# Kernel tuning notes

Measured on AMD Instinct MI355X. Metric: run time of the kernel, lower is better.

The kernel has to match this reference:

```python
import jax, jax.numpy as jnp
import numpy as np

DN = ('NCHW', 'OIHW', 'NCHW')

def conv(x, w, b, stride, pad):
    y = jax.lax.conv_general_dilated(x, w, (stride, stride), ((pad, pad), (pad, pad)), dimension_numbers=DN)
    return y + b[None, :, None, None]

def conv_transpose(x, w, b, stride, pad):
    # w has torch ConvTranspose2d layout (Cin, Cout, kh, kw)
    k = w.shape[2]
    w_f = jnp.transpose(w[:, :, ::-1, ::-1], (1, 0, 2, 3))  # -> OIHW, spatially flipped
    p = k - 1 - pad
    y = jax.lax.conv_general_dilated(x, w_f, (1, 1), ((p, p), (p, p)), lhs_dilation=(stride, stride), dimension_numbers=DN)
    return y + b[None, :, None, None]

def setup_inputs() -> dict:
    key = jax.random.key(0)
    ks = jax.random.split(key, 16)
    K, D = 512, 64
    s = 0.05
    inp = {
        'x': jax.random.uniform(ks[0], (32, 3, 256, 256), dtype=jnp.float32),
        'enc_w1': jax.random.normal(ks[1], (32, 3, 4, 4), jnp.float32) * s,
        'enc_b1': jnp.zeros((32,), jnp.float32),
        'enc_w2': jax.random.normal(ks[2], (64, 32, 4, 4), jnp.float32) * s,
        'enc_b2': jnp.zeros((64,), jnp.float32),
        'enc_w3': jax.random.normal(ks[3], (D, 64, 3, 3), jnp.float32) * s,
        'enc_b3': jnp.zeros((D,), jnp.float32),
        'codebook': jax.random.uniform(ks[4], (K, D), jnp.float32, -1.0 / K, 1.0 / K),
        'dec_w1': jax.random.normal(ks[5], (D, 64, 4, 4), jnp.float32) * s,   # ConvT (Cin,Cout,k,k)
        'dec_b1': jnp.zeros((64,), jnp.float32),
        'dec_w2': jax.random.normal(ks[6], (64, 32, 4, 4), jnp.float32) * s,  # ConvT
        'dec_b2': jnp.zeros((32,), jnp.float32),
        'dec_w3': jax.random.normal(ks[7], (3, 32, 3, 3), jnp.float32) * s,
        'dec_b3': jnp.zeros((3,), jnp.float32),
    }
    return inp

COMMITMENT_COST = 0.25

def reference(x, enc_w1, enc_b1, enc_w2, enc_b2, enc_w3, enc_b3, codebook,
              dec_w1, dec_b1, dec_w2, dec_b2, dec_w3, dec_b3):
    sg = jax.lax.stop_gradient
    # encoder
    h = jax.nn.relu(conv(x, enc_w1, enc_b1, 2, 1))
    h = jax.nn.relu(conv(h, enc_w2, enc_b2, 2, 1))
    z = conv(h, enc_w3, enc_b3, 1, 1)  # [B, D, H/4, W/4]
    # vector quantizer
    D = codebook.shape[1]
    z_perm = jnp.transpose(z, (0, 2, 3, 1))  # BHWD
    flat = z_perm.reshape(-1, D)  # [N, D]
    dist = jnp.sum(flat * flat, axis=1, keepdims=True) - 2.0 * (flat @ codebook.T) + jnp.sum(codebook * codebook, axis=1)  # [N, K]
    idx = jnp.argmin(dist, axis=1)
    q = codebook[idx].reshape(z_perm.shape)
    q = jnp.transpose(q, (0, 3, 1, 2))  # BDHW
    vq_loss = jnp.mean((sg(q) - z) ** 2) + COMMITMENT_COST * jnp.mean((q - sg(z)) ** 2)
    q_st = z + sg(q - z)  # straight-through
    # decoder
    h = jax.nn.relu(conv_transpose(q_st, dec_w1, dec_b1, 2, 1))
    h = jax.nn.relu(conv_transpose(h, dec_w2, dec_b2, 2, 1))
    recon = jax.nn.sigmoid(conv(h, dec_w3, dec_b3, 1, 1))
    return recon, vq_loss
```

## Files before the change

kernel.cpp:

```cpp
#include <hip/hip_runtime.h>

typedef unsigned short u16;
typedef unsigned int u32;
typedef __attribute__((ext_vector_type(8))) short bf16x8;
typedef __attribute__((ext_vector_type(4))) float f32x4;

#define MFMA(a, b, c) __builtin_amdgcn_mfma_f32_16x16x32_bf16(a, b, c, 0, 0, 0)

__device__ __forceinline__ float b2f(u32 lo16) {
  union { u32 i; float f; } v; v.i = lo16 << 16; return v.f;
}
__device__ __forceinline__ u16 f2b(float f) {
  union { float f; u32 i; } v; v.f = f;
  return (u16)((v.i + 0x7fffu + ((v.i >> 16) & 1u)) >> 16);
}
__device__ __forceinline__ u16 f2bt(float f) {
  union { float f; u32 i; } v; v.f = f;
  return (u16)(v.i >> 16);
}
__device__ __forceinline__ bf16x8 ld8(const u16* p) { return *(const bf16x8*)p; }

__global__ void prep_k(const float* __restrict__ ew1, const float* __restrict__ ew2,
                       const float* __restrict__ ew3, const float* __restrict__ dw1,
                       const float* __restrict__ dw2, const float* __restrict__ dw3,
                       const float* __restrict__ cb,
                       float* W1, u16* Bp2, u16* Bp3, u16* BpT1, u16* BpT2,
                       u16* Bpd3, u16* Bpvq, float* cnorm, float* loss) {
  int tid = blockIdx.x * blockDim.x + threadIdx.x;
  int nth = gridDim.x * blockDim.x;
  for (int i = tid; i < 1536; i += nth) {
    int oc = i & 31; int r = i >> 5; int kw = r & 3; r >>= 2; int kh = r & 3; int ic = r >> 2;
    W1[i] = ew1[((oc*3 + ic)*4 + kh)*4 + kw];
  }
  for (int i = tid; i < 32768; i += nth) {
    int j = i & 7, li = (i >> 3) & 63, nt = (i >> 9) & 3, t = i >> 11;
    int ic = 8*(li >> 4) + j, oc = 16*nt + (li & 15), kh = t >> 2, kw = t & 3;
    Bp2[i] = f2b(ew2[((oc*32 + ic)*4 + kh)*4 + kw]);
  }
  for (int i = tid; i < 36864; i += nth) {
    int j = i & 7, li = (i >> 3) & 63, nt = (i >> 9) & 3, kc = (i >> 11) & 1, t = i >> 12;
    int ic = 32*kc + 8*(li >> 4) + j, oc = 16*nt + (li & 15), kh = t / 3, kw = t % 3;
    Bp3[i] = f2b(ew3[((oc*64 + ic)*3 + kh)*3 + kw]);
  }
  for (int i = tid; i < 65536; i += nth) {
    int j = i & 7, li = (i >> 3) & 63, nt = (i >> 9) & 3, kc = (i >> 11) & 1,
        t = (i >> 12) & 3, p = i >> 14;
    int a = p >> 1, b = p & 1;
    int ky = (1 - a) + 2*(t >> 1), kx = (1 - b) + 2*(t & 1);
    int ic = 32*kc + 8*(li >> 4) + j, oc = 16*nt + (li & 15);
    BpT1[i] = f2b(dw1[((ic*64 + oc)*4 + ky)*4 + kx]);
  }
  for (int i = tid; i < 32768; i += nth) {
    int j = i & 7, li = (i >> 3) & 63, mt = (i >> 9) & 1, kc = (i >> 10) & 1,
        t = (i >> 11) & 3, p = i >> 13;
    int a = p >> 1, b = p & 1;
    int ky = (1 - a) + 2*(t >> 1), kx = (1 - b) + 2*(t & 1);
    int oc = 16*mt + (li & 15);
    int ic = 32*kc + 8*(li >> 4) + j;
    BpT2[i] = f2b(dw2[((ic*32 + oc)*4 + ky)*4 + kx]);
  }
  for (int i = tid; i < 4608; i += nth) {
    int j = i & 7, li = (i >> 3) & 63, t = i >> 9;
    int n = li & 15, ic = 8*(li >> 4) + j, kh = t / 3, kw = t % 3;
    Bpd3[i] = (n < 3) ? f2b(dw3[((n*32 + ic)*3 + kh)*3 + kw]) : (u16)0;
  }
  for (int i = tid; i < 32768; i += nth) {
    int j = i & 7, li = (i >> 3) & 63, nt = (i >> 9) & 31, kc = i >> 14;
    int d = 32*kc + 8*(li >> 4) + j, code = 16*nt + (li & 15);
    Bpvq[i] = f2b(cb[code*64 + d]);
  }
  for (int k = tid; k < 512; k += nth) {
    float s = 0.f;
    for (int d = 0; d < 64; ++d) { float c = cb[k*64 + d]; s += c*c; }
    cnorm[k] = s;
  }
  if (tid == 0) *loss = 0.f;
}

__global__ __launch_bounds__(256) void conv1_k(
    const float* __restrict__ x, const float* __restrict__ W1,
    const float* __restrict__ b1, u16* __restrict__ h1) {
  __shared__ float ins[3*18*36];
  int Tx = blockIdx.x, Ty = blockIdx.y, b = blockIdx.z;
  int tid = threadIdx.x;
  for (int i = tid; i < 3*18*36; i += 256) {
    int c = i % 36; int r = (i / 36) % 18; int ic = i / 648;
    int iy = 16*Ty - 1 + r, ix = 32*Tx - 2 + c;
    float v = 0.f;
    if ((unsigned)iy < 256u && (unsigned)ix < 256u)
      v = x[((size_t)(b*3 + ic)*256 + iy)*256 + ix];
    ins[i] = v;
  }
  __syncthreads();
  int posg = tid & 31, ocg = tid >> 5;
  int Y = posg >> 2, Xg = posg & 3;
  int oc0 = ocg * 4;
  float acc[4][4];
#pragma unroll
  for (int j = 0; j < 4; ++j) { float bv = b1[oc0 + j];
#pragma unroll
    for (int e = 0; e < 4; ++e) acc[j][e] = bv; }
  for (int ic = 0; ic < 3; ++ic)
#pragma unroll
    for (int kh = 0; kh < 4; ++kh) {
      const float* row = &ins[ic*648 + (2*Y + kh)*36 + 8*Xg];
      float win[12];
#pragma unroll
      for (int t = 0; t < 12; ++t) win[t] = row[t];
#pragma unroll
      for (int kw = 0; kw < 4; ++kw) {
        const float* wp = &W1[((ic*4 + kh)*4 + kw)*32 + oc0];
        float w0 = wp[0], w1 = wp[1], w2 = wp[2], w3 = wp[3];
#pragma unroll
        for (int e = 0; e < 4; ++e) {
          float v = win[2*e + kw + 1];
          acc[0][e] += w0*v; acc[1][e] += w1*v; acc[2][e] += w2*v; acc[3][e] += w3*v;
        }
      }
    }
  int oy = 8*Ty + Y;
  int oxb = 16*Tx + 4*Xg;
#pragma unroll
  for (int e = 0; e < 4; ++e) {
    u16* op = &h1[((size_t)(b*128 + oy)*128 + oxb + e)*32 + oc0];
#pragma unroll
    for (int j = 0; j < 4; ++j) op[j] = f2b(fmaxf(acc[j][e], 0.f));
  }
}

__global__ __launch_bounds__(256) void conv2_k(
    const u16* __restrict__ h1, const u16* __restrict__ Bp2,
    const float* __restrict__ eb2, u16* __restrict__ h2) {
  __shared__ u16 lds[2448*8];
  int Tx = blockIdx.x, Ty = blockIdx.y, img = blockIdx.z;
  int tid = threadIdx.x;
  for (int i = tid; i < 2448; i += 256) {
    int c = i & 3; int x = (i >> 2) % 34; int row = (i >> 2) / 34;
    int iy = 16*Ty - 1 + row, ix = 32*Tx - 1 + x;
    f32x4 v = {0,0,0,0};
    if ((unsigned)iy < 128u && (unsigned)ix < 128u)
      v = *(const f32x4*)(h1 + (((size_t)(img*128 + iy)*128 + ix)*32 + c*8));
    *(f32x4*)(lds + ((row*4 + c)*34 + x)*8) = v;
  }
  __syncthreads();
  int w = tid >> 6, l = tid & 63, lg = l >> 4, lc = l & 15;
  f32x4 acc[2][4];
#pragma unroll
  for (int nt = 0; nt < 4; ++nt) {
    float bv = eb2[nt*16 + lc];
    acc[0][nt] = (f32x4){bv,bv,bv,bv}; acc[1][nt] = (f32x4){bv,bv,bv,bv};
  }
#pragma unroll
  for (int t = 0; t < 16; ++t) {
    int kh = t >> 2, kw = t & 3;
    bf16x8 a0 = ld8(lds + (((2*w + kh)*4 + lg)*34 + 2*lc + kw)*8);
    bf16x8 a1 = ld8(lds + (((2*(w+4) + kh)*4 + lg)*34 + 2*lc + kw)*8);
    const u16* bp = Bp2 + t*2048 + l*8;
    bf16x8 b0 = ld8(bp), b1 = ld8(bp + 512), b2v = ld8(bp + 1024), b3v = ld8(bp + 1536);
    acc[0][0] = MFMA(a0, b0, acc[0][0]); acc[0][1] = MFMA(a0, b1, acc[0][1]);
    acc[0][2] = MFMA(a0, b2v, acc[0][2]); acc[0][3] = MFMA(a0, b3v, acc[0][3]);
    acc[1][0] = MFMA(a1, b0, acc[1][0]); acc[1][1] = MFMA(a1, b1, acc[1][1]);
    acc[1][2] = MFMA(a1, b2v, acc[1][2]); acc[1][3] = MFMA(a1, b3v, acc[1][3]);
  }
#pragma unroll
  for (int m = 0; m < 2; ++m) {
    int oy = 8*Ty + w + m*4;
#pragma unroll
    for (int nt = 0; nt < 4; ++nt)
#pragma unroll
      for (int r = 0; r < 4; ++r) {
        int e = 4*lg + r;
        h2[((size_t)(img*64 + oy)*64 + 16*Tx + e)*64 + nt*16 + lc] =
            f2b(fmaxf(acc[m][nt][r], 0.f));
      }
  }
}

__global__ __launch_bounds__(256) void conv3e_k(
    const u16* __restrict__ h2, const u16* __restrict__ Bp3,
    const float* __restrict__ eb3, u16* __restrict__ z) {
  __shared__ u16 lds[1440*8];
  int Tx = blockIdx.x, Ty = blockIdx.y, img = blockIdx.z;
  int tid = threadIdx.x;
  for (int i = tid; i < 1440; i += 256) {
    int c = i & 7; int x = (i >> 3) % 18; int row = (i >> 3) / 18;
    int iy = 8*Ty - 1 + row, ix = 16*Tx - 1 + x;
    f32x4 v = {0,0,0,0};
    if ((unsigned)iy < 64u && (unsigned)ix < 64u)
      v = *(const f32x4*)(h2 + (((size_t)(img*64 + iy)*64 + ix)*64 + c*8));
    *(f32x4*)(lds + ((row*8 + c)*18 + x)*8) = v;
  }
  __syncthreads();
  int w = tid >> 6, l = tid & 63, lg = l >> 4, lc = l & 15;
  f32x4 acc[2][4];
#pragma unroll
  for (int nt = 0; nt < 4; ++nt) {
    float bv = eb3[nt*16 + lc];
    acc[0][nt] = (f32x4){bv,bv,bv,bv}; acc[1][nt] = (f32x4){bv,bv,bv,bv};
  }
#pragma unroll
  for (int t = 0; t < 9; ++t) {
    int kh = t / 3, kw = t % 3;
#pragma unroll
    for (int kc = 0; kc < 2; ++kc) {
      bf16x8 a0 = ld8(lds + (((w + kh)*8 + kc*4 + lg)*18 + lc + kw)*8);
      bf16x8 a1 = ld8(lds + (((w + 4 + kh)*8 + kc*4 + lg)*18 + lc + kw)*8);
      const u16* bp = Bp3 + (t*2 + kc)*2048 + l*8;
      bf16x8 b0 = ld8(bp), b1 = ld8(bp + 512), b2v = ld8(bp + 1024), b3v = ld8(bp + 1536);
      acc[0][0] = MFMA(a0, b0, acc[0][0]); acc[0][1] = MFMA(a0, b1, acc[0][1]);
      acc[0][2] = MFMA(a0, b2v, acc[0][2]); acc[0][3] = MFMA(a0, b3v, acc[0][3]);
      acc[1][0] = MFMA(a1, b0, acc[1][0]); acc[1][1] = MFMA(a1, b1, acc[1][1]);
      acc[1][2] = MFMA(a1, b2v, acc[1][2]); acc[1][3] = MFMA(a1, b3v, acc[1][3]);
    }
  }
#pragma unroll
  for (int m = 0; m < 2; ++m) {
    int oy = 8*Ty + w + m*4;
#pragma unroll
    for (int nt = 0; nt < 4; ++nt)
#pragma unroll
      for (int r = 0; r < 4; ++r) {
        int e = 4*lg + r;
        z[((size_t)(img*64 + oy)*64 + 16*Tx + e)*64 + nt*16 + lc] = f2b(acc[m][nt][r]);
      }
  }
}

__global__ __launch_bounds__(256) void vqm_k(
    const u16* __restrict__ z, const u16* __restrict__ Bpvq,
    const float* __restrict__ cnorm, const float* __restrict__ cbf,
    u16* __restrict__ q, float* __restrict__ loss) {
  __shared__ u16 cbl[32768];
  __shared__ float cnl[512];
  __shared__ int idxl[64];
  __shared__ float red[256];
  int tid = threadIdx.x;
  for (int i = tid; i < 4096; i += 256)
    *(f32x4*)(cbl + i*8) = *(const f32x4*)(Bpvq + i*8);
  for (int i = tid; i < 512; i += 256) cnl[i] = cnorm[i];
  __syncthreads();
  int w = tid >> 6, l = tid & 63, lg = l >> 4, lc = l & 15;
  int wglobal = blockIdx.x*4 + w;
  float lsum = 0.f;
  for (int it = 0; it < 2; ++it) {
    int mf = wglobal + it*4096;
    size_t P = (size_t)mf * 16;
    bf16x8 a0 = ld8(z + (P + lc)*64 + lg*8);
    bf16x8 a1 = ld8(z + (P + lc)*64 + 32 + lg*8);
    float best[4] = {1e30f, 1e30f, 1e30f, 1e30f};
    int bidx[4] = {0, 0, 0, 0};
    for (int nt = 0; nt < 32; ++nt) {
      f32x4 acc = {0,0,0,0};
      acc = MFMA(a0, ld8(cbl + (nt*64 + l)*8), acc);
      acc = MFMA(a1, ld8(cbl + ((32 + nt)*64 + l)*8), acc);
      float cn = cnl[nt*16 + lc];
      int code = nt*16 + lc;
#pragma unroll
      for (int r = 0; r < 4; ++r) {
        float dist = cn - 2.f*acc[r];
        if (dist < best[r]) { best[r] = dist; bidx[r] = code; }
      }
    }
#pragma unroll
    for (int r = 0; r < 4; ++r) {
      float b = best[r]; int bi = bidx[r];
      for (int m = 1; m < 16; m <<= 1) {
        float ob = __shfl_xor(b, m);
        int oi = __shfl_xor(bi, m);
        if (ob < b || (ob == b && oi < bi)) { b = ob; bi = oi; }
      }
      if (lc == 0) idxl[w*16 + lg*4 + r] = bi;
    }
    int m = lc, ch0 = lg*16;
    int id = idxl[w*16 + m];
    const float* crow = cbf + (size_t)id*64 + ch0;
    const u16* zp = z + (P + m)*64 + ch0;
    u32* qp = (u32*)(q + (P + m)*64 + ch0);
#pragma unroll
    for (int c = 0; c < 16; c += 2) {
      float c0 = crow[c], c1 = crow[c+1];
      float d0 = c0 - b2f(zp[c]), d1 = c1 - b2f(zp[c+1]);
      lsum += d0*d0 + d1*d1;
      qp[c >> 1] = (u32)f2bt(c0) | ((u32)f2bt(c1) << 16);
    }
  }
  red[tid] = lsum;
  __syncthreads();
  for (int s = 128; s > 0; s >>= 1) {
    if (tid < s) red[tid] += red[tid + s];
    __syncthreads();
  }
  if (tid == 0) atomicAdd(loss, red[0] * (1.25f / 8388608.f));
}

__global__ __launch_bounds__(256) void convt1_k(
    const u16* __restrict__ q, const u16* __restrict__ BpT1,
    const float* __restrict__ db1, u16* __restrict__ d1) {
  __shared__ u16 lds[864*8];
  int Tx = blockIdx.x, Ty = blockIdx.y, img = blockIdx.z;
  int X0 = 16*Tx, P0 = 4*Ty;
  int tid = threadIdx.x;
  for (int i = tid; i < 864; i += 256) {
    int c = i & 7; int x = (i >> 3) % 18; int row = (i >> 3) / 18;
    int iy = P0 - 1 + row, ix = X0 - 1 + x;
    f32x4 v = {0,0,0,0};
    if ((unsigned)iy < 64u && (unsigned)ix < 64u)
      v = *(const f32x4*)(q + (((size_t)(img*64 + iy)*64 + ix)*64 + c*8));
    *(f32x4*)(lds + ((row*8 + c)*18 + x)*8) = v;
  }
  __syncthreads();
  int w = tid >> 6, l = tid & 63, lg = l >> 4, lc = l & 15;
  int a = w & 1, bp_ = w >> 1;
  f32x4 acc[4][4];
#pragma unroll
  for (int nt = 0; nt < 4; ++nt) {
    float bv = db1[nt*16 + lc];
#pragma unroll
    for (int m = 0; m < 4; ++m) acc[m][nt] = (f32x4){bv,bv,bv,bv};
  }
  const u16* bbase = BpT1 + (size_t)(a*2 + bp_)*16384;
#pragma unroll
  for (int t = 0; t < 4; ++t) {
    int kyi = t >> 1, kxi = t & 1;
#pragma unroll
    for (int kc = 0; kc < 2; ++kc) {
      const u16* bp = bbase + (t*2 + kc)*2048 + l*8;
      bf16x8 b0 = ld8(bp), b1 = ld8(bp + 512), b2v = ld8(bp + 1024), b3v = ld8(bp + 1536);
      int xg = lc + bp_ - kxi + 1;
#pragma unroll
      for (int m = 0; m < 4; ++m) {
        int rowg = m + a - kyi + 1;
        bf16x8 av = ld8(lds + ((rowg*8 + kc*4 + lg)*18 + xg)*8);
        acc[m][0] = MFMA(av, b0, acc[m][0]);
        acc[m][1] = MFMA(av, b1, acc[m][1]);
        acc[m][2] = MFMA(av, b2v, acc[m][2]);
        acc[m][3] = MFMA(av, b3v, acc[m][3]);
      }
    }
  }
#pragma unroll
  for (int m = 0; m < 4; ++m) {
    int oy = 2*(P0 + m) + a;
#pragma unroll
    for (int nt = 0; nt < 4; ++nt)
#pragma unroll
      for (int r = 0; r < 4; ++r) {
        int e = 4*lg + r;
        int ox = 2*(X0 + e) + bp_;
        d1[((size_t)(img*128 + oy)*128 + ox)*64 + nt*16 + lc] =
            f2bt(fmaxf(acc[m][nt][r], 0.f));
      }
  }
}

__global__ __launch_bounds__(256) void tail_k(
    const u16* __restrict__ d1, const u16* __restrict__ BpT2,
    const float* __restrict__ db2, const u16* __restrict__ Bpd3,
    const float* __restrict__ db3, float* __restrict__ out) {
  __shared__ u16 d1s[680*8];
  __shared__ u16 d2q[10240];
  int Tx = blockIdx.x, Ty = blockIdx.y, img = blockIdx.z;
  int DX0 = 30*Tx - 1, DY0 = 6*Ty - 1;
  int IYB = 3*Ty, IXB = 15*Tx;
  int tid = threadIdx.x;
  bool edge = (Tx == 0) | (Tx == 8) | (Ty == 0) | (Ty == 42);
  for (int i = tid; i < 680; i += 256) {
    int x = i % 17; int rc = i / 17; int c = rc & 7; int row = rc >> 3;
    int iy = IYB - 1 + row, ix = IXB - 1 + x;
    f32x4 v = {0,0,0,0};
    if ((unsigned)iy < 128u && (unsigned)ix < 128u)
      v = *(const f32x4*)(d1 + (((size_t)(img*128 + iy)*128 + ix)*64 + c*8));
    *(f32x4*)(d1s + ((row*8 + c)*17 + x)*8) = v;
  }
  __syncthreads();
  int w = tid >> 6, l = tid & 63, lg = l >> 4, lc = l & 15;
  {
    int a = w & 1, b = w >> 1;
    f32x4 acc[4][2];
#pragma unroll
    for (int mt = 0; mt < 2; ++mt) {
      f32x4 bv = *(const f32x4*)(db2 + 16*mt + 4*lg);
#pragma unroll
      for (int m = 0; m < 4; ++m) acc[m][mt] = bv;
    }
    const u16* bbase = BpT2 + (size_t)(a*2 + b)*8192;
#pragma unroll
    for (int kxi = 0; kxi < 2; ++kxi) {
      int xg = lc - kxi + 1;
#pragma unroll
      for (int kc = 0; kc < 2; ++kc) {
        bf16x8 av[5];
#pragma unroll
        for (int rr = 0; rr < 5; ++rr)
          av[rr] = ld8(d1s + ((rr*8 + kc*4 + lg)*17 + xg)*8);
#pragma unroll
        for (int kyi = 0; kyi < 2; ++kyi) {
          int t = kyi*2 + kxi;
          const u16* wb = bbase + (t*2 + kc)*1024 + l*8;
          bf16x8 w0 = ld8(wb), w1 = ld8(wb + 512);
#pragma unroll
          for (int m = 0; m < 4; ++m) {
            acc[m][0] = MFMA(w0, av[m + 1 - kyi], acc[m][0]);
            acc[m][1] = MFMA(w1, av[m + 1 - kyi], acc[m][1]);
          }
        }
      }
    }
    int base = (a*2 + b)*2560 + lc*40 + 4*lg;
    if (!edge) {
#pragma unroll
      for (int m = 0; m < 4; ++m)
#pragma unroll
        for (int mt = 0; mt < 2; ++mt) {
          f32x4 v = acc[m][mt];
          u32 lo = (u32)f2bt(fmaxf(v[0], 0.f)) | ((u32)f2bt(fmaxf(v[1], 0.f)) << 16);
          u32 hi = (u32)f2bt(fmaxf(v[2], 0.f)) | ((u32)f2bt(fmaxf(v[3], 0.f)) << 16);
          *(uint2*)(d2q + base + m*640 + mt*16) = (uint2){lo, hi};
        }
    } else {
      int oxc = b ? DX0 : DX0 + 1;
      bool cm = (unsigned)(oxc + 2*lc) < 256u;
      int oyc = a ? DY0 : DY0 + 1;
#pragma unroll
      for (int m = 0; m < 4; ++m) {
        bool ok = ((unsigned)(oyc + 2*m) < 256u) && cm;
#pragma unroll
        for (int mt = 0; mt < 2; ++mt) {
          f32x4 v = acc[m][mt];
          u32 lo = 0, hi = 0;
          if (ok) {
            lo = (u32)f2bt(fmaxf(v[0], 0.f)) | ((u32)f2bt(fmaxf(v[1], 0.f)) << 16);
            hi = (u32)f2bt(fmaxf(v[2], 0.f)) | ((u32)f2bt(fmaxf(v[3], 0.f)) << 16);
          }
          *(uint2*)(d2q + base + m*640 + mt*16) = (uint2){lo, hi};
        }
      }
    }
  }
  __syncthreads();
  bf16x8 bw[9];
#pragma unroll
  for (int t = 0; t < 9; ++t) bw[t] = ld8(Bpd3 + t*512 + l*8);
  float bv3 = (lc < 3) ? db3[lc] : 0.f;
#pragma unroll
  for (int i = 0; i < 3; ++i) {
    int u = w + 4*i;
    int yy = u >> 1, xf = u & 1;
    int gy = DY0 + 1 + yy;
    int cOff[3];
#pragma unroll
    for (int kw = 0; kw < 3; ++kw) {
      int lx = xf*16 + lc + kw; if (lx > 31) lx = 31;
      cOff[kw] = (1 - (lx & 1))*2560 + (lx >> 1)*40 + 8*lg;
    }
    f32x4 acc = {bv3, bv3, bv3, bv3};
#pragma unroll
    for (int kh = 0; kh < 3; ++kh) {
      int ly = yy + kh;
      int rOff = (1 - (ly & 1))*5120 + (ly >> 1)*640;
#pragma unroll
      for (int kw = 0; kw < 3; ++kw)
        acc = MFMA(ld8(d2q + rOff + cOff[kw]), bw[kh*3 + kw], acc);
    }
    if (lc < 3) {
      if (!edge) {
#pragma unroll
        for (int r = 0; r < 4; ++r) {
          int xi = xf*16 + 4*lg + r;
          if (xi < 30)
            out[((size_t)(img*3 + lc)*256 + gy)*256 + DX0 + 1 + xi] =
                __builtin_amdgcn_rcpf(1.f + __expf(-acc[r]));
        }
      } else if ((unsigned)gy < 256u) {
#pragma unroll
        for (int r = 0; r < 4; ++r) {
          int xi = xf*16 + 4*lg + r;
          int gx = DX0 + 1 + xi;
          if (xi < 30 && (unsigned)gx < 256u)
            out[((size_t)(img*3 + lc)*256 + gy)*256 + gx] =
                __builtin_amdgcn_rcpf(1.f + __expf(-acc[r]));
        }
      }
    }
  }
}

extern "C" void kernel_launch(void* const* d_in, const int* in_sizes, int n_in,
                              void* d_out, int out_size, void* d_ws, size_t ws_size,
                              hipStream_t stream) {
  const float* x   = (const float*)d_in[0];
  const float* ew1 = (const float*)d_in[1];
  const float* eb1 = (const float*)d_in[2];
  const float* ew2 = (const float*)d_in[3];
  const float* eb2 = (const float*)d_in[4];
  const float* ew3 = (const float*)d_in[5];
  const float* eb3 = (const float*)d_in[6];
  const float* cb  = (const float*)d_in[7];
  const float* dw1 = (const float*)d_in[8];
  const float* db1 = (const float*)d_in[9];
  const float* dw2 = (const float*)d_in[10];
  const float* db2 = (const float*)d_in[11];
  const float* dw3 = (const float*)d_in[12];
  const float* db3 = (const float*)d_in[13];
  float* out = (float*)d_out;

  char* ws = (char*)d_ws;
  const size_t MB = 1048576;
  u16* h1 = (u16*)ws;
  u16* q  = (u16*)ws;
  u16* d1 = (u16*)(ws + 16*MB);
  u16* h2 = (u16*)(ws + 32*MB);
  u16* z  = (u16*)(ws + 48*MB);
  char* wp = ws + 80*MB;
  float* W1   = (float*)wp;  wp += 6144;
  u16*  Bp2   = (u16*)wp;    wp += 65536;
  u16*  Bp3   = (u16*)wp;    wp += 73728;
  u16*  BpT1  = (u16*)wp;    wp += 131072;
  u16*  BpT2  = (u16*)wp;    wp += 65536;
  u16*  Bpd3  = (u16*)wp;    wp += 9216;
  u16*  Bpvq  = (u16*)wp;    wp += 65536;
  float* cnorm = (float*)wp; wp += 2048;
  float* loss = out + 6291456;

  prep_k<<<64, 256, 0, stream>>>(ew1, ew2, ew3, dw1, dw2, dw3, cb,
                                 W1, Bp2, Bp3, BpT1, BpT2, Bpd3, Bpvq, cnorm, loss);
  conv1_k<<<dim3(8, 16, 32), 256, 0, stream>>>(x, W1, eb1, h1);
  conv2_k<<<dim3(4, 8, 32), 256, 0, stream>>>(h1, Bp2, eb2, h2);
  conv3e_k<<<dim3(4, 8, 32), 256, 0, stream>>>(h2, Bp3, eb3, z);
  vqm_k<<<1024, 256, 0, stream>>>(z, Bpvq, cnorm, cb, q, loss);
  convt1_k<<<dim3(4, 16, 32), 256, 0, stream>>>(q, BpT1, db1, d1);
  tail_k<<<dim3(9, 43, 32), 256, 0, stream>>>(d1, BpT2, db2, Bpd3, db3, out);
}
```

Before: 292.9 us.

## Swap MFMA operands so accumulators hold channels and pack bf16 stores

The weight and activation operands of the MFMA calls in conv2, conv3, and the first transposed conv are swapped, so each lane's four accumulator values are consecutive output channels rather than consecutive pixels. The epilogues then write 8-byte packed vectors instead of scattered 2-byte stores. Bias loads become vector loads. All float-to-bf16 conversions, including the tail kernel's and the VQ output's, now use the hardware v_cvt_pk_bf16_f32 instruction, which changes rounding from truncation or manual RNE to hardware rounding.

```diff
diff --git a/kernel.cpp b/kernel.cpp
--- a/kernel.cpp
+++ b/kernel.cpp
@@ -14,9 +14,8 @@
   union { float f; u32 i; } v; v.f = f;
   return (u16)((v.i + 0x7fffu + ((v.i >> 16) & 1u)) >> 16);
 }
-__device__ __forceinline__ u16 f2bt(float f) {
-  union { float f; u32 i; } v; v.f = f;
-  return (u16)(v.i >> 16);
+__device__ __forceinline__ u32 pk2(float a, float b) {
+  u32 r; asm("v_cvt_pk_bf16_f32 %0, %1, %2" : "=v"(r) : "v"(a), "v"(b)); return r;
 }
 __device__ __forceinline__ bf16x8 ld8(const u16* p) { return *(const bf16x8*)p; }
 
@@ -122,9 +121,9 @@
   int oxb = 16*Tx + 4*Xg;
 #pragma unroll
   for (int e = 0; e < 4; ++e) {
-    u16* op = &h1[((size_t)(b*128 + oy)*128 + oxb + e)*32 + oc0];
-#pragma unroll
-    for (int j = 0; j < 4; ++j) op[j] = f2b(fmaxf(acc[j][e], 0.f));
+    u32 lo = pk2(fmaxf(acc[0][e], 0.f), fmaxf(acc[1][e], 0.f));
+    u32 hi = pk2(fmaxf(acc[2][e], 0.f), fmaxf(acc[3][e], 0.f));
+    *(uint2*)&h1[((size_t)(b*128 + oy)*128 + oxb + e)*32 + oc0] = (uint2){lo, hi};
   }
 }
 
@@ -146,9 +145,9 @@
   int w = tid >> 6, l = tid & 63, lg = l >> 4, lc = l & 15;
   f32x4 acc[2][4];
 #pragma unroll
-  for (int nt = 0; nt < 4; ++nt) {
-    float bv = eb2[nt*16 + lc];
-    acc[0][nt] = (f32x4){bv,bv,bv,bv}; acc[1][nt] = (f32x4){bv,bv,bv,bv};
+  for (int mt = 0; mt < 4; ++mt) {
+    f32x4 bv = *(const f32x4*)(eb2 + mt*16 + 4*lg);
+    acc[0][mt] = bv; acc[1][mt] = bv;
   }
 #pragma unroll
   for (int t = 0; t < 16; ++t) {
@@ -156,23 +155,23 @@
     bf16x8 a0 = ld8(lds + (((2*w + kh)*4 + lg)*34 + 2*lc + kw)*8);
     bf16x8 a1 = ld8(lds + (((2*(w+4) + kh)*4 + lg)*34 + 2*lc + kw)*8);
     const u16* bp = Bp2 + t*2048 + l*8;
-    bf16x8 b0 = ld8(bp), b1 = ld8(bp + 512), b2v = ld8(bp + 1024), b3v = ld8(bp + 1536);
-    acc[0][0] = MFMA(a0, b0, acc[0][0]); acc[0][1] = MFMA(a0, b1, acc[0][1]);
-    acc[0][2] = MFMA(a0, b2v, acc[0][2]); acc[0][3] = MFMA(a0, b3v, acc[0][3]);
-    acc[1][0] = MFMA(a1, b0, acc[1][0]); acc[1][1] = MFMA(a1, b1, acc[1][1]);
-    acc[1][2] = MFMA(a1, b2v, acc[1][2]); acc[1][3] = MFMA(a1, b3v, acc[1][3]);
+    bf16x8 w0 = ld8(bp), w1 = ld8(bp + 512), w2 = ld8(bp + 1024), w3 = ld8(bp + 1536);
+    acc[0][0] = MFMA(w0, a0, acc[0][0]); acc[0][1] = MFMA(w1, a0, acc[0][1]);
+    acc[0][2] = MFMA(w2, a0, acc[0][2]); acc[0][3] = MFMA(w3, a0, acc[0][3]);
+    acc[1][0] = MFMA(w0, a1, acc[1][0]); acc[1][1] = MFMA(w1, a1, acc[1][1]);
+    acc[1][2] = MFMA(w2, a1, acc[1][2]); acc[1][3] = MFMA(w3, a1, acc[1][3]);
   }
 #pragma unroll
   for (int m = 0; m < 2; ++m) {
     int oy = 8*Ty + w + m*4;
-#pragma unroll
-    for (int nt = 0; nt < 4; ++nt)
-#pragma unroll
-      for (int r = 0; r < 4; ++r) {
-        int e = 4*lg + r;
-        h2[((size_t)(img*64 + oy)*64 + 16*Tx + e)*64 + nt*16 + lc] =
-            f2b(fmaxf(acc[m][nt][r], 0.f));
-      }
+    u16* base = h2 + ((size_t)(img*64 + oy)*64 + 16*Tx + lc)*64 + 4*lg;
+#pragma unroll
+    for (int mt = 0; mt < 4; ++mt) {
+      f32x4 v = acc[m][mt];
+      u32 lo = pk2(fmaxf(v[0], 0.f), fmaxf(v[1], 0.f));
+      u32 hi = pk2(fmaxf(v[2], 0.f), fmaxf(v[3], 0.f));
+      *(uint2*)(base + mt*16) = (uint2){lo, hi};
+    }
   }
 }
 
@@ -194,9 +193,9 @@
   int w = tid >> 6, l = tid & 63, lg = l >> 4, lc = l & 15;
   f32x4 acc[2][4];
 #pragma unroll
-  for (int nt = 0; nt < 4; ++nt) {
-    float bv = eb3[nt*16 + lc];
-    acc[0][nt] = (f32x4){bv,bv,bv,bv}; acc[1][nt] = (f32x4){bv,bv,bv,bv};
+  for (int mt = 0; mt < 4; ++mt) {
+    f32x4 bv = *(const f32x4*)(eb3 + mt*16 + 4*lg);
+    acc[0][mt] = bv; acc[1][mt] = bv;
   }
 #pragma unroll
   for (int t = 0; t < 9; ++t) {
@@ -206,23 +205,22 @@
       bf16x8 a0 = ld8(lds + (((w + kh)*8 + kc*4 + lg)*18 + lc + kw)*8);
       bf16x8 a1 = ld8(lds + (((w + 4 + kh)*8 + kc*4 + lg)*18 + lc + kw)*8);
       const u16* bp = Bp3 + (t*2 + kc)*2048 + l*8;
-      bf16x8 b0 = ld8(bp), b1 = ld8(bp + 512), b2v = ld8(bp + 1024), b3v = ld8(bp + 1536);
-      acc[0][0] = MFMA(a0, b0, acc[0][0]); acc[0][1] = MFMA(a0, b1, acc[0][1]);
-      acc[0][2] = MFMA(a0, b2v, acc[0][2]); acc[0][3] = MFMA(a0, b3v, acc[0][3]);
-      acc[1][0] = MFMA(a1, b0, acc[1][0]); acc[1][1] = MFMA(a1, b1, acc[1][1]);
-      acc[1][2] = MFMA(a1, b2v, acc[1][2]); acc[1][3] = MFMA(a1, b3v, acc[1][3]);
+      bf16x8 w0 = ld8(bp), w1 = ld8(bp + 512), w2 = ld8(bp + 1024), w3 = ld8(bp + 1536);
+      acc[0][0] = MFMA(w0, a0, acc[0][0]); acc[0][1] = MFMA(w1, a0, acc[0][1]);
+      acc[0][2] = MFMA(w2, a0, acc[0][2]); acc[0][3] = MFMA(w3, a0, acc[0][3]);
+      acc[1][0] = MFMA(w0, a1, acc[1][0]); acc[1][1] = MFMA(w1, a1, acc[1][1]);
+      acc[1][2] = MFMA(w2, a1, acc[1][2]); acc[1][3] = MFMA(w3, a1, acc[1][3]);
     }
   }
 #pragma unroll
   for (int m = 0; m < 2; ++m) {
     int oy = 8*Ty + w + m*4;
-#pragma unroll
-    for (int nt = 0; nt < 4; ++nt)
-#pragma unroll
-      for (int r = 0; r < 4; ++r) {
-        int e = 4*lg + r;
-        z[((size_t)(img*64 + oy)*64 + 16*Tx + e)*64 + nt*16 + lc] = f2b(acc[m][nt][r]);
-      }
+    u16* base = z + ((size_t)(img*64 + oy)*64 + 16*Tx + lc)*64 + 4*lg;
+#pragma unroll
+    for (int mt = 0; mt < 4; ++mt) {
+      f32x4 v = acc[m][mt];
+      *(uint2*)(base + mt*16) = (uint2){pk2(v[0], v[1]), pk2(v[2], v[3])};
+    }
   }
 }
 
@@ -281,7 +279,7 @@
       float c0 = crow[c], c1 = crow[c+1];
       float d0 = c0 - b2f(zp[c]), d1 = c1 - b2f(zp[c+1]);
       lsum += d0*d0 + d1*d1;
-      qp[c >> 1] = (u32)f2bt(c0) | ((u32)f2bt(c1) << 16);
+      qp[c >> 1] = pk2(c0, c1);
     }
   }
   red[tid] = lsum;
@@ -313,10 +311,10 @@
   int a = w & 1, bp_ = w >> 1;
   f32x4 acc[4][4];
 #pragma unroll
-  for (int nt = 0; nt < 4; ++nt) {
-    float bv = db1[nt*16 + lc];
-#pragma unroll
-    for (int m = 0; m < 4; ++m) acc[m][nt] = (f32x4){bv,bv,bv,bv};
+  for (int mt = 0; mt < 4; ++mt) {
+    f32x4 bv = *(const f32x4*)(db1 + mt*16 + 4*lg);
+#pragma unroll
+    for (int m = 0; m < 4; ++m) acc[m][mt] = bv;
   }
   const u16* bbase = BpT1 + (size_t)(a*2 + bp_)*16384;
 #pragma unroll
@@ -325,31 +323,31 @@
 #pragma unroll
     for (int kc = 0; kc < 2; ++kc) {
       const u16* bp = bbase + (t*2 + kc)*2048 + l*8;
-      bf16x8 b0 = ld8(bp), b1 = ld8(bp + 512), b2v = ld8(bp + 1024), b3v = ld8(bp + 1536);
+      bf16x8 w0 = ld8(bp), w1 = ld8(bp + 512), w2 = ld8(bp + 1024), w3 = ld8(bp + 1536);
       int xg = lc + bp_ - kxi + 1;
 #pragma unroll
       for (int m = 0; m < 4; ++m) {
         int rowg = m + a - kyi + 1;
-        bf16x8 av = ld8(lds + ((rowg*8 + kc*4 + lg)*18 + xg)*8);
-        acc[m][0] = MFMA(av, b0, acc[m][0]);
-        acc[m][1] = MFMA(av, b1, acc[m][1]);
-        acc[m][2] = MFMA(av, b2v, acc[m][2]);
-        acc[m][3] = MFMA(av, b3v, acc[m][3]);
-      }
-    }
-  }
+        bf16x8 dv = ld8(lds + ((rowg*8 + kc*4 + lg)*18 + xg)*8);
+        acc[m][0] = MFMA(w0, dv, acc[m][0]);
+        acc[m][1] = MFMA(w1, dv, acc[m][1]);
+        acc[m][2] = MFMA(w2, dv, acc[m][2]);
+        acc[m][3] = MFMA(w3, dv, acc[m][3]);
+      }
+    }
+  }
+  int ox = 2*(X0 + lc) + bp_;
 #pragma unroll
   for (int m = 0; m < 4; ++m) {
     int oy = 2*(P0 + m) + a;
-#pragma unroll
-    for (int nt = 0; nt < 4; ++nt)
-#pragma unroll
-      for (int r = 0; r < 4; ++r) {
-        int e = 4*lg + r;
-        int ox = 2*(X0 + e) + bp_;
-        d1[((size_t)(img*128 + oy)*128 + ox)*64 + nt*16 + lc] =
-            f2bt(fmaxf(acc[m][nt][r], 0.f));
-      }
+    u16* base = d1 + ((size_t)(img*128 + oy)*128 + ox)*64 + 4*lg;
+#pragma unroll
+    for (int mt = 0; mt < 4; ++mt) {
+      f32x4 v = acc[m][mt];
+      u32 lo = pk2(fmaxf(v[0], 0.f), fmaxf(v[1], 0.f));
+      u32 hi = pk2(fmaxf(v[2], 0.f), fmaxf(v[3], 0.f));
+      *(uint2*)(base + mt*16) = (uint2){lo, hi};
+    }
   }
 }
 
@@ -413,8 +411,8 @@
 #pragma unroll
         for (int mt = 0; mt < 2; ++mt) {
           f32x4 v = acc[m][mt];
-          u32 lo = (u32)f2bt(fmaxf(v[0], 0.f)) | ((u32)f2bt(fmaxf(v[1], 0.f)) << 16);
-          u32 hi = (u32)f2bt(fmaxf(v[2], 0.f)) | ((u32)f2bt(fmaxf(v[3], 0.f)) << 16);
+          u32 lo = pk2(fmaxf(v[0], 0.f), fmaxf(v[1], 0.f));
+          u32 hi = pk2(fmaxf(v[2], 0.f), fmaxf(v[3], 0.f));
           *(uint2*)(d2q + base + m*640 + mt*16) = (uint2){lo, hi};
         }
     } else {
@@ -429,8 +427,8 @@
           f32x4 v = acc[m][mt];
           u32 lo = 0, hi = 0;
           if (ok) {
-            lo = (u32)f2bt(fmaxf(v[0], 0.f)) | ((u32)f2bt(fmaxf(v[1], 0.f)) << 16);
-            hi = (u32)f2bt(fmaxf(v[2], 0.f)) | ((u32)f2bt(fmaxf(v[3], 0.f)) << 16);
+            lo = pk2(fmaxf(v[0], 0.f), fmaxf(v[1], 0.f));
+            hi = pk2(fmaxf(v[2], 0.f), fmaxf(v[3], 0.f));
           }
           *(uint2*)(d2q + base + m*640 + mt*16) = (uint2){lo, hi};
         }
```

After: 298.9 us. +2.0%, slower.
